# Performance work log

Hardware: AMD Instinct MI355X
Metric: run time of the kernel (lower is better)

Reference implementation:

```python
import jax, jax.numpy as jnp
import numpy as np

N = 100000   # nodes
E = 1600000  # edges
C = 128      # channels
EPS = 1e-5   # BatchNorm eps (PyG gnn.BatchNorm default)


def gcn_conv(x, W, b, src, dst, n):
    """PyG GCNConv: linear -> sym-normalized aggregation with self-loops -> bias."""
    h = x @ W                                      # [N, C]
    # degree with self-loops: in-degree at dst + 1
    deg = jnp.zeros((n,), h.dtype).at[dst].add(jnp.ones((), h.dtype)) + 1.0
    dinv = jax.lax.rsqrt(deg)                      # [N]
    norm = dinv[src] * dinv[dst]                   # [E]
    agg = jnp.zeros_like(h).at[dst].add(h[src] * norm[:, None])
    agg = agg + h * (dinv * dinv)[:, None]         # self-loop contribution
    return agg + b


def batch_norm(x, gamma, beta):
    """Training-mode BatchNorm over the node dimension (per-channel)."""
    mu = jnp.mean(x, axis=0)
    var = jnp.mean(jnp.square(x - mu), axis=0)     # biased variance
    return (x - mu) * jax.lax.rsqrt(var + EPS) * gamma + beta


def setup_inputs() -> dict:
    key = jax.random.key(0)
    ks = jax.random.split(key, 8)
    s = 1.0 / np.sqrt(C)
    x = jax.random.normal(ks[0], (N, C), dtype=jnp.float32)
    edge_index = jax.random.randint(ks[1], (2, E), 0, N, dtype=jnp.int64)
    W1 = jax.random.uniform(ks[2], (C, C), jnp.float32, -s, s)
    b1 = jax.random.uniform(ks[3], (C,), jnp.float32, -s, s)
    W2 = jax.random.uniform(ks[4], (C, C), jnp.float32, -s, s)
    b2 = jax.random.uniform(ks[5], (C,), jnp.float32, -s, s)
    gamma2 = jnp.ones((C,), jnp.float32)
    beta2 = jnp.zeros((C,), jnp.float32)
    return {"x": x, "W1": W1, "b1": b1, "W2": W2, "b2": b2,
            "gamma2": gamma2, "beta2": beta2, "edge_index": edge_index}


def reference(x, W1, b1, W2, b2, gamma2, beta2, edge_index):
    src, dst = edge_index[0], edge_index[1]
    identity = x
    # NOTE: original forward applies batch_norm2 after BOTH convs (batch_norm1 unused).
    h = jax.nn.relu(batch_norm(gcn_conv(x, W1, b1, src, dst, N), gamma2, beta2))
    h = batch_norm(gcn_conv(h, W2, b2, src, dst, N), gamma2, beta2)
    return jax.nn.relu(h + identity)
```

## Files before the change

### kernel.cpp

```cpp
#include <hip/hip_runtime.h>

#define N_NODES 100000
#define EDGES   1600000
#define CH      128
#define BN_EPS  1e-5f

#define BINS     782
#define CHUNKS   256
#define CHUNK_E  (EDGES / CHUNKS)
#define HM       (BINS * CHUNKS)
#define SCAN_NB  (HM / 256)
#define NREP     64

typedef __attribute__((ext_vector_type(8))) __bf16 bf16x8;
typedef __attribute__((ext_vector_type(4))) __bf16 bf16x4;
typedef __attribute__((ext_vector_type(2))) __bf16 bf16x2;
typedef __attribute__((ext_vector_type(4))) float  f32x4;

__global__ __launch_bounds__(256) void histo_kernel(const int* __restrict__ dst,
                                                    int* __restrict__ histo_g) {
    __shared__ int h[BINS];
    int t = threadIdx.x;
    for (int b = t; b < BINS; b += 256) h[b] = 0;
    __syncthreads();
    int base = blockIdx.x * CHUNK_E;
    for (int i = t; i < CHUNK_E; i += 256)
        atomicAdd(&h[dst[base + i] >> 7], 1);
    __syncthreads();
    for (int b = t; b < BINS; b += 256)
        histo_g[b * CHUNKS + blockIdx.x] = h[b];
}

__global__ __launch_bounds__(256) void scan1(const int* __restrict__ in,
                                             int* __restrict__ scanned,
                                             int* __restrict__ blocksum) {
    __shared__ int sh[2][256];
    int t = threadIdx.x;
    int i = blockIdx.x * 256 + t;
    int v = in[i];
    sh[0][t] = v;
    __syncthreads();
    int pp = 0;
    #pragma unroll
    for (int off = 1; off < 256; off <<= 1) {
        int val = sh[pp][t] + ((t >= off) ? sh[pp][t - off] : 0);
        sh[1 - pp][t] = val;
        pp = 1 - pp;
        __syncthreads();
    }
    int incl = sh[pp][t];
    scanned[i] = incl - v;
    if (t == 255) blocksum[blockIdx.x] = incl;
}

__global__ __launch_bounds__(1024) void scan2(int* __restrict__ blocksum) {
    __shared__ int sh[2][1024];
    int t = threadIdx.x;
    int v = (t < SCAN_NB) ? blocksum[t] : 0;
    sh[0][t] = v;
    __syncthreads();
    int pp = 0;
    #pragma unroll
    for (int off = 1; off < 1024; off <<= 1) {
        int val = sh[pp][t] + ((t >= off) ? sh[pp][t - off] : 0);
        sh[1 - pp][t] = val;
        pp = 1 - pp;
        __syncthreads();
    }
    if (t < SCAN_NB) blocksum[t] = sh[pp][t] - v;
}

__global__ __launch_bounds__(256) void scan3(int* __restrict__ scanned,
                                             const int* __restrict__ blocksum) {
    int i = blockIdx.x * 256 + threadIdx.x;
    scanned[i] += blocksum[blockIdx.x];
    if (i == HM - 1) scanned[HM] = EDGES;
}

__global__ __launch_bounds__(256) void place_kernel(const int* __restrict__ src,
                                                    const int* __restrict__ dst,
                                                    const int* __restrict__ scanned,
                                                    int* __restrict__ binned) {
    __shared__ int cur[BINS];
    int t = threadIdx.x;
    for (int b = t; b < BINS; b += 256)
        cur[b] = scanned[b * CHUNKS + blockIdx.x];
    __syncthreads();
    int base = blockIdx.x * CHUNK_E;
    for (int i = t; i < CHUNK_E; i += 256) {
        int d = dst[base + i];
        int s = src[base + i];
        int pos = atomicAdd(&cur[d >> 7], 1);
        binned[pos] = (s << 7) | (d & 127);
    }
}

__global__ __launch_bounds__(256) void bin_csr(const int* __restrict__ binned,
                                               const int* __restrict__ scanned,
                                               int* __restrict__ srcs,
                                               int* __restrict__ rowptr,
                                               float* __restrict__ dinv) {
    __shared__ int cnt[128];
    __shared__ int sc[2][128];
    __shared__ int base[128];
    __shared__ int cur[128];
    const int t = threadIdx.x;
    const int bin = blockIdx.x;
    if (t < 128) { cnt[t] = 0; cur[t] = 0; }
    __syncthreads();
    const int beg = scanned[bin * CHUNKS];
    const int end = scanned[bin * CHUNKS + CHUNKS];
    for (int e = beg + t; e < end; e += 256)
        atomicAdd(&cnt[binned[e] & 127], 1);
    __syncthreads();
    if (t < 128) sc[0][t] = cnt[t];
    __syncthreads();
    int pp = 0;
    #pragma unroll
    for (int off = 1; off < 128; off <<= 1) {
        if (t < 128) sc[1 - pp][t] = sc[pp][t] + ((t >= off) ? sc[pp][t - off] : 0);
        pp = 1 - pp;
        __syncthreads();
    }
    if (t < 128) {
        base[t] = beg + sc[pp][t] - cnt[t];
        int n = (bin << 7) + t;
        if (n < N_NODES) {
            rowptr[n] = base[t];
            dinv[n] = rsqrtf((float)cnt[t] + 1.0f);
        }
    }
    if (bin == 0 && t == 0) rowptr[N_NODES] = EDGES;
    __syncthreads();
    for (int e = beg + t; e < end; e += 256) {
        int p = binned[e];
        int dl = p & 127;
        int pos = base[dl] + atomicAdd(&cur[dl], 1);
        srcs[pos] = p >> 7;
    }
}

__global__ __launch_bounds__(256) void wtrans2(const float* __restrict__ W1,
                                               __bf16* __restrict__ Wt1,
                                               const float* __restrict__ W2,
                                               __bf16* __restrict__ Wt2) {
    int b = blockIdx.x;
    const float* W = (b < 64) ? W1 : W2;
    __bf16* Wt = (b < 64) ? Wt1 : Wt2;
    int idx = (b & 63) * 256 + threadIdx.x;
    int n = idx >> 7, k = idx & 127;
    Wt[idx] = (__bf16)W[k * 128 + n];
}

__global__ __launch_bounds__(256) void gemm_f32(const float* __restrict__ A,
                                                const __bf16* __restrict__ Wt,
                                                const float* __restrict__ dinv,
                                                __bf16* __restrict__ hs) {
    const int wave = threadIdx.x >> 6;
    const int rt = blockIdx.x * 4 + wave;
    if (rt >= N_NODES / 16) return;
    const int lane = threadIdx.x & 63;
    const int ln = lane & 15;
    const int quad = lane >> 4;
    const int arow = rt * 16 + ln;

    f32x4 acc[8];
    #pragma unroll
    for (int ct = 0; ct < 8; ++ct) acc[ct] = (f32x4){0.f, 0.f, 0.f, 0.f};

    #pragma unroll
    for (int k0 = 0; k0 < 128; k0 += 32) {
        const int k = k0 + quad * 8;
        float4 a0 = *(const float4*)(A + (size_t)arow * CH + k);
        float4 a1 = *(const float4*)(A + (size_t)arow * CH + k + 4);
        bf16x8 af;
        af[0] = (__bf16)a0.x; af[1] = (__bf16)a0.y;
        af[2] = (__bf16)a0.z; af[3] = (__bf16)a0.w;
        af[4] = (__bf16)a1.x; af[5] = (__bf16)a1.y;
        af[6] = (__bf16)a1.z; af[7] = (__bf16)a1.w;
        #pragma unroll
        for (int ct = 0; ct < 8; ++ct) {
            bf16x8 bfrag = *(const bf16x8*)(Wt + (size_t)(ct * 16 + ln) * CH + k);
            acc[ct] = __builtin_amdgcn_mfma_f32_16x16x32_bf16(af, bfrag, acc[ct], 0, 0, 0);
        }
    }

    #pragma unroll
    for (int r = 0; r < 4; ++r) {
        const int row_r = rt * 16 + quad * 4 + r;
        const float dr = dinv[row_r];
        __bf16* orow = hs + (size_t)row_r * CH + ln;
        #pragma unroll
        for (int ct = 0; ct < 8; ++ct)
            orow[ct * 16] = (__bf16)(acc[ct][r] * dr);
    }
}

__global__ __launch_bounds__(256) void gemm_bn(const __bf16* __restrict__ A,
                                               const __bf16* __restrict__ Wt,
                                               const float* __restrict__ dinv,
                                               const float* __restrict__ scale,
                                               const float* __restrict__ shift,
                                               __bf16* __restrict__ hs) {
    const int wave = threadIdx.x >> 6;
    const int rt = blockIdx.x * 4 + wave;
    if (rt >= N_NODES / 16) return;
    const int lane = threadIdx.x & 63;
    const int ln = lane & 15;
    const int quad = lane >> 4;
    const int arow = rt * 16 + ln;

    f32x4 acc[8];
    #pragma unroll
    for (int ct = 0; ct < 8; ++ct) acc[ct] = (f32x4){0.f, 0.f, 0.f, 0.f};

    #pragma unroll
    for (int k0 = 0; k0 < 128; k0 += 32) {
        const int k = k0 + quad * 8;
        bf16x8 av = *(const bf16x8*)(A + (size_t)arow * CH + k);
        bf16x8 af;
        #pragma unroll
        for (int j = 0; j < 8; ++j)
            af[j] = (__bf16)fmaxf(fmaf((float)av[j], scale[k + j], shift[k + j]), 0.f);
        #pragma unroll
        for (int ct = 0; ct < 8; ++ct) {
            bf16x8 bfrag = *(const bf16x8*)(Wt + (size_t)(ct * 16 + ln) * CH + k);
            acc[ct] = __builtin_amdgcn_mfma_f32_16x16x32_bf16(af, bfrag, acc[ct], 0, 0, 0);
        }
    }

    #pragma unroll
    for (int r = 0; r < 4; ++r) {
        const int row_r = rt * 16 + quad * 4 + r;
        const float dr = dinv[row_r];
        __bf16* orow = hs + (size_t)row_r * CH + ln;
        #pragma unroll
        for (int ct = 0; ct < 8; ++ct)
            orow[ct * 16] = (__bf16)(acc[ct][r] * dr);
    }
}

__global__ __launch_bounds__(256) void gather_agg(const __bf16* __restrict__ hs,
                                                  const int* __restrict__ srcs,
                                                  const int* __restrict__ rowptr,
                                                  const float* __restrict__ dinv,
                                                  __bf16* __restrict__ agg,
                                                  float* __restrict__ gpart) {
    __shared__ float red[4][64][4];
    const int wave = threadIdx.x >> 6;
    const int c2 = threadIdx.x & 63;
    const bf16x2* hp = (const bf16x2*)hs;

    float s0 = 0.f, ss0 = 0.f, s1 = 0.f, ss1 = 0.f;

    #pragma unroll
    for (int it = 0; it < 2; ++it) {
        const int n = __builtin_amdgcn_readfirstlane(blockIdx.x * 8 + wave * 2 + it);
        const int beg = rowptr[n];
        const int end = rowptr[n + 1];
        bf16x2 sv = hp[(size_t)n * 64 + c2];
        float ax = (float)sv[0], ay = (float)sv[1];
        int j = beg;
        for (; j + 8 <= end; j += 8) {
            int e0 = srcs[j + 0], e1 = srcs[j + 1], e2 = srcs[j + 2], e3 = srcs[j + 3];
            int e4 = srcs[j + 4], e5 = srcs[j + 5], e6 = srcs[j + 6], e7 = srcs[j + 7];
            bf16x2 v0 = hp[(size_t)e0 * 64 + c2];
            bf16x2 v1 = hp[(size_t)e1 * 64 + c2];
            bf16x2 v2 = hp[(size_t)e2 * 64 + c2];
            bf16x2 v3 = hp[(size_t)e3 * 64 + c2];
            bf16x2 v4 = hp[(size_t)e4 * 64 + c2];
            bf16x2 v5 = hp[(size_t)e5 * 64 + c2];
            bf16x2 v6 = hp[(size_t)e6 * 64 + c2];
            bf16x2 v7 = hp[(size_t)e7 * 64 + c2];
            ax += (((float)v0[0] + (float)v1[0]) + ((float)v2[0] + (float)v3[0]))
                + (((float)v4[0] + (float)v5[0]) + ((float)v6[0] + (float)v7[0]));
            ay += (((float)v0[1] + (float)v1[1]) + ((float)v2[1] + (float)v3[1]))
                + (((float)v4[1] + (float)v5[1]) + ((float)v6[1] + (float)v7[1]));
        }
        for (; j < end; ++j) {
            bf16x2 v = hp[(size_t)srcs[j] * 64 + c2];
            ax += (float)v[0];
            ay += (float)v[1];
        }
        float d = dinv[n];
        float ox = ax * d, oy = ay * d;
        bf16x2 o; o[0] = (__bf16)ox; o[1] = (__bf16)oy;
        ((bf16x2*)agg)[(size_t)n * 64 + c2] = o;
        s0 += ox; ss0 += ox * ox;
        s1 += oy; ss1 += oy * oy;
    }

    f32x4 rv; rv[0] = s0; rv[1] = ss0; rv[2] = s1; rv[3] = ss1;
    *(f32x4*)red[wave][c2] = rv;
    __syncthreads();
    const int t = threadIdx.x;
    float v = red[0][t >> 2][t & 3] + red[1][t >> 2][t & 3] +
              red[2][t >> 2][t & 3] + red[3][t >> 2][t & 3];
    atomicAdd(&gpart[(blockIdx.x & (NREP - 1)) * 256 + t], v);
}

__global__ void bn_final(const float* __restrict__ gpart,
                         const float* __restrict__ gamma,
                         const float* __restrict__ beta,
                         float* __restrict__ scale,
                         float* __restrict__ shift) {
    int c = threadIdx.x;
    int c2 = c >> 1, odd = c & 1;
    float s = 0.f, ss = 0.f;
    for (int r = 0; r < NREP; ++r) {
        s  += gpart[r * 256 + c2 * 4 + 2 * odd];
        ss += gpart[r * 256 + c2 * 4 + 2 * odd + 1];
    }
    const float invN = 1.0f / (float)N_NODES;
    float mu = s * invN;
    float var = ss * invN - mu * mu;
    float sc = gamma[c] * rsqrtf(var + BN_EPS);
    scale[c] = sc;
    shift[c] = beta[c] - mu * sc;
}

__global__ __launch_bounds__(256) void bn_apply_res_relu(const __bf16* __restrict__ v,
                                                         const float* __restrict__ scale,
                                                         const float* __restrict__ shift,
                                                         const float* __restrict__ xin,
                                                         float* __restrict__ outv) {
    int i = blockIdx.x * 256 + threadIdx.x;
    int cg = i & 31;
    bf16x4 a4 = ((const bf16x4*)v)[i];
    float4 r = ((const float4*)xin)[i];
    float4 sc = ((const float4*)scale)[cg];
    float4 sh = ((const float4*)shift)[cg];
    float4 a;
    a.x = fmaxf(fmaf((float)a4[0], sc.x, sh.x) + r.x, 0.f);
    a.y = fmaxf(fmaf((float)a4[1], sc.y, sh.y) + r.y, 0.f);
    a.z = fmaxf(fmaf((float)a4[2], sc.z, sh.z) + r.z, 0.f);
    a.w = fmaxf(fmaf((float)a4[3], sc.w, sh.w) + r.w, 0.f);
    ((float4*)outv)[i] = a;
}

extern "C" void kernel_launch(void* const* d_in, const int* in_sizes, int n_in,
                              void* d_out, int out_size, void* d_ws, size_t ws_size,
                              hipStream_t stream) {
    const float* x      = (const float*)d_in[0];
    const float* W1     = (const float*)d_in[1];
    const float* W2     = (const float*)d_in[3];
    const float* gamma2 = (const float*)d_in[5];
    const float* beta2  = (const float*)d_in[6];
    const int*   ei     = (const int*)d_in[7];
    const int*   srcI   = ei;
    const int*   dstI   = ei + EDGES;
    float* out = (float*)d_out;

    char* ws = (char*)d_ws;
    __bf16* agg      = (__bf16*)(ws);
    __bf16* hs       = (__bf16*)(ws + 25600000);
    int*    binned   = (int*)   (ws + 51200000);
    int*    srcs     = (int*)   (ws + 57600000);
    int*    histo_g  = (int*)   (ws + 64000000);
    int*    scanned  = (int*)   (ws + 64801024);
    int*    blocksum = (int*)   (ws + 65602048);
    float*  dinv     = (float*) (ws + 65605632);
    int*    rowptr   = (int*)   (ws + 66005632);
    __bf16* Wt1      = (__bf16*)(ws + 66405888);
    __bf16* Wt2      = (__bf16*)(ws + 66438656);
    float*  gpart    = (float*) (ws + 66471424);
    float*  scale1   = (float*) (ws + 66536960);
    float*  shift1   = scale1 + 128;
    float*  scale2   = scale1 + 256;
    float*  shift2   = scale1 + 384;

    const int ELEM4_BLOCKS  = (N_NODES * 32) / 256;
    const int GEMM_BLOCKS   = (N_NODES / 16 + 3) / 4;
    const int GATHER_BLOCKS = N_NODES / 8;

    histo_kernel<<<CHUNKS, 256, 0, stream>>>(dstI, histo_g);
    scan1<<<SCAN_NB, 256, 0, stream>>>(histo_g, scanned, blocksum);
    scan2<<<1, 1024, 0, stream>>>(blocksum);
    scan3<<<SCAN_NB, 256, 0, stream>>>(scanned, blocksum);
    place_kernel<<<CHUNKS, 256, 0, stream>>>(srcI, dstI, scanned, binned);
    bin_csr<<<BINS, 256, 0, stream>>>(binned, scanned, srcs, rowptr, dinv);
    wtrans2<<<128, 256, 0, stream>>>(W1, Wt1, W2, Wt2);

    gemm_f32<<<GEMM_BLOCKS, 256, 0, stream>>>(x, Wt1, dinv, hs);
    hipMemsetAsync(gpart, 0, NREP * 256 * sizeof(float), stream);
    gather_agg<<<GATHER_BLOCKS, 256, 0, stream>>>(hs, srcs, rowptr, dinv, agg, gpart);
    bn_final<<<1, 128, 0, stream>>>(gpart, gamma2, beta2, scale1, shift1);

    gemm_bn<<<GEMM_BLOCKS, 256, 0, stream>>>(agg, Wt2, dinv, scale1, shift1, hs);
    hipMemsetAsync(gpart, 0, NREP * 256 * sizeof(float), stream);
    gather_agg<<<GATHER_BLOCKS, 256, 0, stream>>>(hs, srcs, rowptr, dinv, agg, gpart);
    bn_final<<<1, 128, 0, stream>>>(gpart, gamma2, beta2, scale2, shift2);
    bn_apply_res_relu<<<ELEM4_BLOCKS, 256, 0, stream>>>(agg, scale2, shift2, x, out);
}
```

Baseline: 382.9 us.

## Fuse kernels and move dinv scaling into gather to shrink launch chain

Merges the weight transpose with the histogram, and the first GEMM with the first scan pass, into single launches by splitting on block index. The source-side dinv scaling moves from the GEMM epilogue into the gather, so GEMM1 no longer waits for CSR construction. BN finalisation is folded into the consumers (gemm2 and a grid-stride epilogue) through a shared-memory reduction, and the gpart zeroing moves into GEMM blocks instead of memsets. The cost is an extra random dinv load per edge in the gather, and every block redundantly reduces the BN partials.

```diff
diff --git a/kernel.cpp b/kernel.cpp
--- a/kernel.cpp
+++ b/kernel.cpp
@@ -11,46 +11,106 @@
 #define HM       (BINS * CHUNKS)
 #define SCAN_NB  (HM / 256)
 #define NREP     64
+#define GEMM_BLOCKS 1563
 
 typedef __attribute__((ext_vector_type(8))) __bf16 bf16x8;
 typedef __attribute__((ext_vector_type(4))) __bf16 bf16x4;
 typedef __attribute__((ext_vector_type(2))) __bf16 bf16x2;
 typedef __attribute__((ext_vector_type(4))) float  f32x4;
 
-__global__ __launch_bounds__(256) void histo_kernel(const int* __restrict__ dst,
+__global__ __launch_bounds__(256) void wtrans_histo(const float* __restrict__ W1,
+                                                    __bf16* __restrict__ Wt1,
+                                                    const float* __restrict__ W2,
+                                                    __bf16* __restrict__ Wt2,
+                                                    const int* __restrict__ dst,
                                                     int* __restrict__ histo_g) {
-    __shared__ int h[BINS];
+    int b = blockIdx.x;
     int t = threadIdx.x;
-    for (int b = t; b < BINS; b += 256) h[b] = 0;
-    __syncthreads();
-    int base = blockIdx.x * CHUNK_E;
-    for (int i = t; i < CHUNK_E; i += 256)
-        atomicAdd(&h[dst[base + i] >> 7], 1);
-    __syncthreads();
-    for (int b = t; b < BINS; b += 256)
-        histo_g[b * CHUNKS + blockIdx.x] = h[b];
-}
-
-__global__ __launch_bounds__(256) void scan1(const int* __restrict__ in,
-                                             int* __restrict__ scanned,
-                                             int* __restrict__ blocksum) {
-    __shared__ int sh[2][256];
-    int t = threadIdx.x;
-    int i = blockIdx.x * 256 + t;
-    int v = in[i];
-    sh[0][t] = v;
-    __syncthreads();
-    int pp = 0;
-    #pragma unroll
-    for (int off = 1; off < 256; off <<= 1) {
-        int val = sh[pp][t] + ((t >= off) ? sh[pp][t - off] : 0);
-        sh[1 - pp][t] = val;
-        pp = 1 - pp;
+    if (b < 128) {
+        const float* W = (b < 64) ? W1 : W2;
+        __bf16* Wt = (b < 64) ? Wt1 : Wt2;
+        int idx = (b & 63) * 256 + t;
+        int n = idx >> 7, k = idx & 127;
+        Wt[idx] = (__bf16)W[k * 128 + n];
+    } else {
+        __shared__ int h[BINS];
+        int chunk = b - 128;
+        for (int i = t; i < BINS; i += 256) h[i] = 0;
         __syncthreads();
-    }
-    int incl = sh[pp][t];
-    scanned[i] = incl - v;
-    if (t == 255) blocksum[blockIdx.x] = incl;
+        int base = chunk * CHUNK_E;
+        for (int i = t; i < CHUNK_E; i += 256)
+            atomicAdd(&h[dst[base + i] >> 7], 1);
+        __syncthreads();
+        for (int i = t; i < BINS; i += 256)
+            histo_g[i * CHUNKS + chunk] = h[i];
+    }
+}
+
+__global__ __launch_bounds__(256) void gemm1_scan(const float* __restrict__ A,
+                                                  const __bf16* __restrict__ Wt,
+                                                  __bf16* __restrict__ hs,
+                                                  const int* __restrict__ histo_g,
+                                                  int* __restrict__ scanned,
+                                                  int* __restrict__ blocksum,
+                                                  float* __restrict__ gpart1) {
+    const int t = threadIdx.x;
+    if (blockIdx.x < GEMM_BLOCKS) {
+        if (blockIdx.x < NREP) gpart1[blockIdx.x * 256 + t] = 0.f;
+        const int wave = t >> 6;
+        const int rt = blockIdx.x * 4 + wave;
+        if (rt >= N_NODES / 16) return;
+        const int lane = t & 63;
+        const int ln = lane & 15;
+        const int quad = lane >> 4;
+        const int arow = rt * 16 + ln;
+
+        f32x4 acc[8];
+        #pragma unroll
+        for (int ct = 0; ct < 8; ++ct) acc[ct] = (f32x4){0.f, 0.f, 0.f, 0.f};
+
+        #pragma unroll
+        for (int k0 = 0; k0 < 128; k0 += 32) {
+            const int k = k0 + quad * 8;
+            float4 a0 = *(const float4*)(A + (size_t)arow * CH + k);
+            float4 a1 = *(const float4*)(A + (size_t)arow * CH + k + 4);
+            bf16x8 af;
+            af[0] = (__bf16)a0.x; af[1] = (__bf16)a0.y;
+            af[2] = (__bf16)a0.z; af[3] = (__bf16)a0.w;
+            af[4] = (__bf16)a1.x; af[5] = (__bf16)a1.y;
+            af[6] = (__bf16)a1.z; af[7] = (__bf16)a1.w;
+            #pragma unroll
+            for (int ct = 0; ct < 8; ++ct) {
+                bf16x8 bfrag = *(const bf16x8*)(Wt + (size_t)(ct * 16 + ln) * CH + k);
+                acc[ct] = __builtin_amdgcn_mfma_f32_16x16x32_bf16(af, bfrag, acc[ct], 0, 0, 0);
+            }
+        }
+        #pragma unroll
+        for (int r = 0; r < 4; ++r) {
+            const int row_r = rt * 16 + quad * 4 + r;
+            __bf16* orow = hs + (size_t)row_r * CH + ln;
+            #pragma unroll
+            for (int ct = 0; ct < 8; ++ct)
+                orow[ct * 16] = (__bf16)acc[ct][r];
+        }
+    } else {
+        __shared__ int sh[2][256];
+        int sb = blockIdx.x - GEMM_BLOCKS;
+        int i = sb * 256 + t;
+        int v = histo_g[i];
+        sh[0][t] = v;
+        __syncthreads();
+        int pp = 0;
+        #pragma unroll
+        for (int off = 1; off < 256; off <<= 1) {
+            int val = sh[pp][t] + ((t >= off) ? sh[pp][t - off] : 0);
+            sh[1 - pp][t] = val;
+            pp = 1 - pp;
+            __syncthreads();
+        }
+        int incl = sh[pp][t];
+        scanned[i] = incl - v;
+        if (t == 255) blocksum[sb] = incl;
+    }
 }
 
 __global__ __launch_bounds__(1024) void scan2(int* __restrict__ blocksum) {
@@ -140,106 +200,6 @@
     }
 }
 
-__global__ __launch_bounds__(256) void wtrans2(const float* __restrict__ W1,
-                                               __bf16* __restrict__ Wt1,
-                                               const float* __restrict__ W2,
-                                               __bf16* __restrict__ Wt2) {
-    int b = blockIdx.x;
-    const float* W = (b < 64) ? W1 : W2;
-    __bf16* Wt = (b < 64) ? Wt1 : Wt2;
-    int idx = (b & 63) * 256 + threadIdx.x;
-    int n = idx >> 7, k = idx & 127;
-    Wt[idx] = (__bf16)W[k * 128 + n];
-}
-
-__global__ __launch_bounds__(256) void gemm_f32(const float* __restrict__ A,
-                                                const __bf16* __restrict__ Wt,
-                                                const float* __restrict__ dinv,
-                                                __bf16* __restrict__ hs) {
-    const int wave = threadIdx.x >> 6;
-    const int rt = blockIdx.x * 4 + wave;
-    if (rt >= N_NODES / 16) return;
-    const int lane = threadIdx.x & 63;
-    const int ln = lane & 15;
-    const int quad = lane >> 4;
-    const int arow = rt * 16 + ln;
-
-    f32x4 acc[8];
-    #pragma unroll
-    for (int ct = 0; ct < 8; ++ct) acc[ct] = (f32x4){0.f, 0.f, 0.f, 0.f};
-
-    #pragma unroll
-    for (int k0 = 0; k0 < 128; k0 += 32) {
-        const int k = k0 + quad * 8;
-        float4 a0 = *(const float4*)(A + (size_t)arow * CH + k);
-        float4 a1 = *(const float4*)(A + (size_t)arow * CH + k + 4);
-        bf16x8 af;
-        af[0] = (__bf16)a0.x; af[1] = (__bf16)a0.y;
-        af[2] = (__bf16)a0.z; af[3] = (__bf16)a0.w;
-        af[4] = (__bf16)a1.x; af[5] = (__bf16)a1.y;
-        af[6] = (__bf16)a1.z; af[7] = (__bf16)a1.w;
-        #pragma unroll
-        for (int ct = 0; ct < 8; ++ct) {
-            bf16x8 bfrag = *(const bf16x8*)(Wt + (size_t)(ct * 16 + ln) * CH + k);
-            acc[ct] = __builtin_amdgcn_mfma_f32_16x16x32_bf16(af, bfrag, acc[ct], 0, 0, 0);
-        }
-    }
-
-    #pragma unroll
-    for (int r = 0; r < 4; ++r) {
-        const int row_r = rt * 16 + quad * 4 + r;
-        const float dr = dinv[row_r];
-        __bf16* orow = hs + (size_t)row_r * CH + ln;
-        #pragma unroll
-        for (int ct = 0; ct < 8; ++ct)
-            orow[ct * 16] = (__bf16)(acc[ct][r] * dr);
-    }
-}
-
-__global__ __launch_bounds__(256) void gemm_bn(const __bf16* __restrict__ A,
-                                               const __bf16* __restrict__ Wt,
-                                               const float* __restrict__ dinv,
-                                               const float* __restrict__ scale,
-                                               const float* __restrict__ shift,
-                                               __bf16* __restrict__ hs) {
-    const int wave = threadIdx.x >> 6;
-    const int rt = blockIdx.x * 4 + wave;
-    if (rt >= N_NODES / 16) return;
-    const int lane = threadIdx.x & 63;
-    const int ln = lane & 15;
-    const int quad = lane >> 4;
-    const int arow = rt * 16 + ln;
-
-    f32x4 acc[8];
-    #pragma unroll
-    for (int ct = 0; ct < 8; ++ct) acc[ct] = (f32x4){0.f, 0.f, 0.f, 0.f};
-
-    #pragma unroll
-    for (int k0 = 0; k0 < 128; k0 += 32) {
-        const int k = k0 + quad * 8;
-        bf16x8 av = *(const bf16x8*)(A + (size_t)arow * CH + k);
-        bf16x8 af;
-        #pragma unroll
-        for (int j = 0; j < 8; ++j)
-            af[j] = (__bf16)fmaxf(fmaf((float)av[j], scale[k + j], shift[k + j]), 0.f);
-        #pragma unroll
-        for (int ct = 0; ct < 8; ++ct) {
-            bf16x8 bfrag = *(const bf16x8*)(Wt + (size_t)(ct * 16 + ln) * CH + k);
-            acc[ct] = __builtin_amdgcn_mfma_f32_16x16x32_bf16(af, bfrag, acc[ct], 0, 0, 0);
-        }
-    }
-
-    #pragma unroll
-    for (int r = 0; r < 4; ++r) {
-        const int row_r = rt * 16 + quad * 4 + r;
-        const float dr = dinv[row_r];
-        __bf16* orow = hs + (size_t)row_r * CH + ln;
-        #pragma unroll
-        for (int ct = 0; ct < 8; ++ct)
-            orow[ct * 16] = (__bf16)(acc[ct][r] * dr);
-    }
-}
-
 __global__ __launch_bounds__(256) void gather_agg(const __bf16* __restrict__ hs,
                                                   const int* __restrict__ srcs,
                                                   const int* __restrict__ rowptr,
@@ -258,12 +218,15 @@
         const int n = __builtin_amdgcn_readfirstlane(blockIdx.x * 8 + wave * 2 + it);
         const int beg = rowptr[n];
         const int end = rowptr[n + 1];
+        const float d = dinv[n];
         bf16x2 sv = hp[(size_t)n * 64 + c2];
-        float ax = (float)sv[0], ay = (float)sv[1];
+        float ax = d * (float)sv[0], ay = d * (float)sv[1];
         int j = beg;
         for (; j + 8 <= end; j += 8) {
             int e0 = srcs[j + 0], e1 = srcs[j + 1], e2 = srcs[j + 2], e3 = srcs[j + 3];
             int e4 = srcs[j + 4], e5 = srcs[j + 5], e6 = srcs[j + 6], e7 = srcs[j + 7];
+            float d0 = dinv[e0], d1 = dinv[e1], d2 = dinv[e2], d3 = dinv[e3];
+            float d4 = dinv[e4], d5 = dinv[e5], d6 = dinv[e6], d7 = dinv[e7];
             bf16x2 v0 = hp[(size_t)e0 * 64 + c2];
             bf16x2 v1 = hp[(size_t)e1 * 64 + c2];
             bf16x2 v2 = hp[(size_t)e2 * 64 + c2];
@@ -272,17 +235,22 @@
             bf16x2 v5 = hp[(size_t)e5 * 64 + c2];
             bf16x2 v6 = hp[(size_t)e6 * 64 + c2];
             bf16x2 v7 = hp[(size_t)e7 * 64 + c2];
-            ax += (((float)v0[0] + (float)v1[0]) + ((float)v2[0] + (float)v3[0]))
-                + (((float)v4[0] + (float)v5[0]) + ((float)v6[0] + (float)v7[0]));
-            ay += (((float)v0[1] + (float)v1[1]) + ((float)v2[1] + (float)v3[1]))
-                + (((float)v4[1] + (float)v5[1]) + ((float)v6[1] + (float)v7[1]));
+            ax = fmaf(d0, (float)v0[0], ax); ay = fmaf(d0, (float)v0[1], ay);
+            ax = fmaf(d1, (float)v1[0], ax); ay = fmaf(d1, (float)v1[1], ay);
+            ax = fmaf(d2, (float)v2[0], ax); ay = fmaf(d2, (float)v2[1], ay);
+            ax = fmaf(d3, (float)v3[0], ax); ay = fmaf(d3, (float)v3[1], ay);
+            ax = fmaf(d4, (float)v4[0], ax); ay = fmaf(d4, (float)v4[1], ay);
+            ax = fmaf(d5, (float)v5[0], ax); ay = fmaf(d5, (float)v5[1], ay);
+            ax = fmaf(d6, (float)v6[0], ax); ay = fmaf(d6, (float)v6[1], ay);
+            ax = fmaf(d7, (float)v7[0], ax); ay = fmaf(d7, (float)v7[1], ay);
         }
         for (; j < end; ++j) {
-            bf16x2 v = hp[(size_t)srcs[j] * 64 + c2];
-            ax += (float)v[0];
-            ay += (float)v[1];
-        }
-        float d = dinv[n];
+            int e = srcs[j];
+            float de = dinv[e];
+            bf16x2 v = hp[(size_t)e * 64 + c2];
+            ax = fmaf(de, (float)v[0], ax);
+            ay = fmaf(de, (float)v[1], ay);
+        }
         float ox = ax * d, oy = ay * d;
         bf16x2 o; o[0] = (__bf16)ox; o[1] = (__bf16)oy;
         ((bf16x2*)agg)[(size_t)n * 64 + c2] = o;
@@ -299,43 +267,98 @@
     atomicAdd(&gpart[(blockIdx.x & (NREP - 1)) * 256 + t], v);
 }
 
-__global__ void bn_final(const float* __restrict__ gpart,
-                         const float* __restrict__ gamma,
-                         const float* __restrict__ beta,
-                         float* __restrict__ scale,
-                         float* __restrict__ shift) {
-    int c = threadIdx.x;
-    int c2 = c >> 1, odd = c & 1;
-    float s = 0.f, ss = 0.f;
-    for (int r = 0; r < NREP; ++r) {
-        s  += gpart[r * 256 + c2 * 4 + 2 * odd];
-        ss += gpart[r * 256 + c2 * 4 + 2 * odd + 1];
-    }
-    const float invN = 1.0f / (float)N_NODES;
-    float mu = s * invN;
-    float var = ss * invN - mu * mu;
-    float sc = gamma[c] * rsqrtf(var + BN_EPS);
-    scale[c] = sc;
-    shift[c] = beta[c] - mu * sc;
-}
-
-__global__ __launch_bounds__(256) void bn_apply_res_relu(const __bf16* __restrict__ v,
-                                                         const float* __restrict__ scale,
-                                                         const float* __restrict__ shift,
-                                                         const float* __restrict__ xin,
-                                                         float* __restrict__ outv) {
-    int i = blockIdx.x * 256 + threadIdx.x;
-    int cg = i & 31;
-    bf16x4 a4 = ((const bf16x4*)v)[i];
-    float4 r = ((const float4*)xin)[i];
-    float4 sc = ((const float4*)scale)[cg];
-    float4 sh = ((const float4*)shift)[cg];
-    float4 a;
-    a.x = fmaxf(fmaf((float)a4[0], sc.x, sh.x) + r.x, 0.f);
-    a.y = fmaxf(fmaf((float)a4[1], sc.y, sh.y) + r.y, 0.f);
-    a.z = fmaxf(fmaf((float)a4[2], sc.z, sh.z) + r.z, 0.f);
-    a.w = fmaxf(fmaf((float)a4[3], sc.w, sh.w) + r.w, 0.f);
-    ((float4*)outv)[i] = a;
+__device__ __forceinline__ void bn_reduce_lds(const float* __restrict__ gpart,
+                                              const float* __restrict__ gamma,
+                                              const float* __restrict__ beta,
+                                              float* sc_s, float* sh_s) {
+    const int t = threadIdx.x;
+    if (t < 128) {
+        int c2 = t >> 1, odd = t & 1;
+        float s = 0.f, ss = 0.f;
+        for (int r = 0; r < NREP; ++r) {
+            s  += gpart[r * 256 + c2 * 4 + 2 * odd];
+            ss += gpart[r * 256 + c2 * 4 + 2 * odd + 1];
+        }
+        const float invN = 1.0f / (float)N_NODES;
+        float mu = s * invN;
+        float var = ss * invN - mu * mu;
+        float sc = gamma[t] * rsqrtf(var + BN_EPS);
+        sc_s[t] = sc;
+        sh_s[t] = beta[t] - mu * sc;
+    }
+    __syncthreads();
+}
+
+__global__ __launch_bounds__(256) void gemm2_bn(const __bf16* __restrict__ A,
+                                                const __bf16* __restrict__ Wt,
+                                                const float* __restrict__ gpart1,
+                                                const float* __restrict__ gamma,
+                                                const float* __restrict__ beta,
+                                                __bf16* __restrict__ hs,
+                                                float* __restrict__ gpart2) {
+    __shared__ float sc_s[128], sh_s[128];
+    const int t = threadIdx.x;
+    if (blockIdx.x < NREP) gpart2[blockIdx.x * 256 + t] = 0.f;
+    bn_reduce_lds(gpart1, gamma, beta, sc_s, sh_s);
+
+    const int wave = t >> 6;
+    const int rt = blockIdx.x * 4 + wave;
+    if (rt >= N_NODES / 16) return;
+    const int lane = t & 63;
+    const int ln = lane & 15;
+    const int quad = lane >> 4;
+    const int arow = rt * 16 + ln;
+
+    f32x4 acc[8];
+    #pragma unroll
+    for (int ct = 0; ct < 8; ++ct) acc[ct] = (f32x4){0.f, 0.f, 0.f, 0.f};
+
+    #pragma unroll
+    for (int k0 = 0; k0 < 128; k0 += 32) {
+        const int k = k0 + quad * 8;
+        bf16x8 av = *(const bf16x8*)(A + (size_t)arow * CH + k);
+        bf16x8 af;
+        #pragma unroll
+        for (int j = 0; j < 8; ++j)
+            af[j] = (__bf16)fmaxf(fmaf((float)av[j], sc_s[k + j], sh_s[k + j]), 0.f);
+        #pragma unroll
+        for (int ct = 0; ct < 8; ++ct) {
+            bf16x8 bfrag = *(const bf16x8*)(Wt + (size_t)(ct * 16 + ln) * CH + k);
+            acc[ct] = __builtin_amdgcn_mfma_f32_16x16x32_bf16(af, bfrag, acc[ct], 0, 0, 0);
+        }
+    }
+
+    #pragma unroll
+    for (int r = 0; r < 4; ++r) {
+        const int row_r = rt * 16 + quad * 4 + r;
+        __bf16* orow = hs + (size_t)row_r * CH + ln;
+        #pragma unroll
+        for (int ct = 0; ct < 8; ++ct)
+            orow[ct * 16] = (__bf16)acc[ct][r];
+    }
+}
+
+__global__ __launch_bounds__(256) void epilogue_bn(const __bf16* __restrict__ v,
+                                                   const float* __restrict__ gpart2,
+                                                   const float* __restrict__ gamma,
+                                                   const float* __restrict__ beta,
+                                                   const float* __restrict__ xin,
+                                                   float* __restrict__ outv) {
+    __shared__ float sc_s[128], sh_s[128];
+    bn_reduce_lds(gpart2, gamma, beta, sc_s, sh_s);
+
+    const int total4 = N_NODES * 32;
+    for (int i = blockIdx.x * 256 + threadIdx.x; i < total4; i += 2048 * 256) {
+        int cg = i & 31;
+        bf16x4 a4 = ((const bf16x4*)v)[i];
+        float4 r = ((const float4*)xin)[i];
+        float4 a;
+        a.x = fmaxf(fmaf((float)a4[0], sc_s[cg * 4 + 0], sh_s[cg * 4 + 0]) + r.x, 0.f);
+        a.y = fmaxf(fmaf((float)a4[1], sc_s[cg * 4 + 1], sh_s[cg * 4 + 1]) + r.y, 0.f);
+        a.z = fmaxf(fmaf((float)a4[2], sc_s[cg * 4 + 2], sh_s[cg * 4 + 2]) + r.z, 0.f);
+        a.w = fmaxf(fmaf((float)a4[3], sc_s[cg * 4 + 3], sh_s[cg * 4 + 3]) + r.w, 0.f);
+        ((float4*)outv)[i] = a;
+    }
 }
 
 extern "C" void kernel_launch(void* const* d_in, const int* in_sizes, int n_in,
@@ -363,32 +386,21 @@
     int*    rowptr   = (int*)   (ws + 66005632);
     __bf16* Wt1      = (__bf16*)(ws + 66405888);
     __bf16* Wt2      = (__bf16*)(ws + 66438656);
-    float*  gpart    = (float*) (ws + 66471424);
-    float*  scale1   = (float*) (ws + 66536960);
-    float*  shift1   = scale1 + 128;
-    float*  scale2   = scale1 + 256;
-    float*  shift2   = scale1 + 384;
-
-    const int ELEM4_BLOCKS  = (N_NODES * 32) / 256;
-    const int GEMM_BLOCKS   = (N_NODES / 16 + 3) / 4;
+    float*  gpart1   = (float*) (ws + 66471424);
+    float*  gpart2   = (float*) (ws + 66536960);
+
     const int GATHER_BLOCKS = N_NODES / 8;
 
-    histo_kernel<<<CHUNKS, 256, 0, stream>>>(dstI, histo_g);
-    scan1<<<SCAN_NB, 256, 0, stream>>>(histo_g, scanned, blocksum);
+    wtrans_histo<<<128 + CHUNKS, 256, 0, stream>>>(W1, Wt1, W2, Wt2, dstI, histo_g);
+    gemm1_scan<<<GEMM_BLOCKS + SCAN_NB, 256, 0, stream>>>(x, Wt1, hs, histo_g,
+                                                          scanned, blocksum, gpart1);
     scan2<<<1, 1024, 0, stream>>>(blocksum);
     scan3<<<SCAN_NB, 256, 0, stream>>>(scanned, blocksum);
     place_kernel<<<CHUNKS, 256, 0, stream>>>(srcI, dstI, scanned, binned);
     bin_csr<<<BINS, 256, 0, stream>>>(binned, scanned, srcs, rowptr, dinv);
-    wtrans2<<<128, 256, 0, stream>>>(W1, Wt1, W2, Wt2);
-
-    gemm_f32<<<GEMM_BLOCKS, 256, 0, stream>>>(x, Wt1, dinv, hs);
-    hipMemsetAsync(gpart, 0, NREP * 256 * sizeof(float), stream);
-    gather_agg<<<GATHER_BLOCKS, 256, 0, stream>>>(hs, srcs, rowptr, dinv, agg, gpart);
-    bn_final<<<1, 128, 0, stream>>>(gpart, gamma2, beta2, scale1, shift1);
-
-    gemm_bn<<<GEMM_BLOCKS, 256, 0, stream>>>(agg, Wt2, dinv, scale1, shift1, hs);
-    hipMemsetAsync(gpart, 0, NREP * 256 * sizeof(float), stream);
-    gather_agg<<<GATHER_BLOCKS, 256, 0, stream>>>(hs, srcs, rowptr, dinv, agg, gpart);
-    bn_final<<<1, 128, 0, stream>>>(gpart, gamma2, beta2, scale2, shift2);
-    bn_apply_res_relu<<<ELEM4_BLOCKS, 256, 0, stream>>>(agg, scale2, shift2, x, out);
-}
+
+    gather_agg<<<GATHER_BLOCKS, 256, 0, stream>>>(hs, srcs, rowptr, dinv, agg, gpart1);
+    gemm2_bn<<<GEMM_BLOCKS, 256, 0, stream>>>(agg, Wt2, gpart1, gamma2, beta2, hs, gpart2);
+    gather_agg<<<GATHER_BLOCKS, 256, 0, stream>>>(hs, srcs, rowptr, dinv, agg, gpart2);
+    epilogue_bn<<<2048, 256, 0, stream>>>(agg, gpart2, gamma2, beta2, x, out);
+}
```

Result: slower. 394.6 us (+3.0%).
